# Kernel optimization log

Hardware: AMD Instinct MI355X
Metric: run time of the kernel (lower is better)

The kernel has to match this reference:

```python
import jax, jax.numpy as jnp
import numpy as np

POS = np.array([[0,3,0.5],[0,3,1.5],[0,3,2.5],[0,3,3.5],[0,3,4.5],[0,3,5.5],[1,0,0],[1,6,6],[2,0,6],[2,6,0],[3,0,0],[3,6,6],[4,0,6],[4,6,0],[5,0,0],[5,6,6],[6,0,6],[6,6,0],[7,0,0],[7,6,6],[8,0,6],[8,6,0],[9,0,0],[9,6,6],[10,0,6],[10,6,0],[11,0,0],[11,6,6],[12,0,6],[12,6,0],[13,0,0],[13,6,6],[14,0,6],[14,6,0],[15,0,0],[15,6,6],[16,0,6],[16,6,0],[17,0.5,0.5],[17,3,0.5],[17,5.5,0.5],[17,0.5,3],[17,3,3],[17,5.5,3],[17,0.5,5.5],[17,3,5.5],[17,5.5,5.5]], dtype=np.float32)  # (47,3) fixed buffer

B, S, D, H, FF, HID = 512, 47, 32, 4, 2048, 256

def _ln(x, w, b, eps=1e-5):
    mu = jnp.mean(x, -1, keepdims=True)
    var = jnp.mean((x - mu) ** 2, -1, keepdims=True)
    return (x - mu) * jax.lax.rsqrt(var + eps) * w + b

def _encoder_layer(h, wi, bi, wo, bo, l1w, l1b, f1w, f1b, f2w, f2b, l2w, l2b):
    # torch post-norm TransformerEncoderLayer; batch_first=False => attention over axis 0
    L, N, E = h.shape
    Dh = E // H
    qkv = h @ wi.T + bi                                  # (L,N,3E)
    q, k, v = jnp.split(qkv, 3, axis=-1)
    q = q.reshape(L, N, H, Dh); k = k.reshape(L, N, H, Dh); v = v.reshape(L, N, H, Dh)
    scores = jnp.einsum('lnhd,mnhd->nhlm', q, k) * (1.0 / np.sqrt(Dh))  # (N,H,L,L)
    a = jax.nn.softmax(scores, axis=-1)
    o = jnp.einsum('nhlm,mnhd->lnhd', a, v).reshape(L, N, E)
    h = _ln(h + (o @ wo.T + bo), l1w, l1b)
    ff = jax.nn.relu(h @ f1w.T + f1b) @ f2w.T + f2b
    return _ln(h + ff, l2w, l2b)

def setup_inputs():
    key = jax.random.key(0)
    ks = list(jax.random.split(key, 24))
    rn = lambda k, s, sc=0.05: jax.random.normal(k, s, jnp.float32) * sc
    return dict(
        x=jax.random.normal(ks[0], (B, S), jnp.float32),
        w_in=rn(ks[1], (D, 1)), b_in=rn(ks[2], (D,)),
        w_pos=rn(ks[3], (D, 3)), b_pos=rn(ks[4], (D,)),
        cls_token=rn(ks[5], (1, 1, D), 1.0),
        attn_in_w=rn(ks[6], (2, 3 * D, D)), attn_in_b=rn(ks[7], (2, 3 * D)),
        attn_out_w=rn(ks[8], (2, D, D)), attn_out_b=rn(ks[9], (2, D)),
        ln1_w=jnp.ones((2, D)), ln1_b=jnp.zeros((2, D)),
        ff1_w=rn(ks[10], (2, FF, D)), ff1_b=rn(ks[11], (2, FF)),
        ff2_w=rn(ks[12], (2, D, FF)), ff2_b=rn(ks[13], (2, D)),
        ln2_w=jnp.ones((2, D)), ln2_b=jnp.zeros((2, D)),
        out_w=rn(ks[14], (1, D)), out_b=rn(ks[15], (1,)),
        mlp_w0=rn(ks[16], (HID, S)), mlp_b0=rn(ks[17], (HID,)),
        mlp_w1=rn(ks[18], (HID, HID)), mlp_b1=rn(ks[19], (HID,)),
        mlp_w2=rn(ks[20], (1, HID)), mlp_b2=rn(ks[21], (1,)),
    )

def reference(x, w_in, b_in, w_pos, b_pos, cls_token, attn_in_w, attn_in_b, attn_out_w, attn_out_b, ln1_w, ln1_b, ff1_w, ff1_b, ff2_w, ff2_b, ln2_w, ln2_b, out_w, out_b, mlp_w0, mlp_b0, mlp_w1, mlp_b1, mlp_w2, mlp_b2):
    Bn = x.shape[0]
    h = x[..., None] * w_in[:, 0] + b_in                 # Linear(1,D): (B,S,D)
    h = h + (jnp.asarray(POS) @ w_pos.T + b_pos)         # pos projection (S,D)
    cls = jnp.broadcast_to(cls_token, (Bn, 1, D))
    h = jnp.concatenate([cls, h], axis=1)                # (B,S+1,D)
    for i in range(2):
        h = _encoder_layer(h, attn_in_w[i], attn_in_b[i], attn_out_w[i], attn_out_b[i], ln1_w[i], ln1_b[i], ff1_w[i], ff1_b[i], ff2_w[i], ff2_b[i], ln2_w[i], ln2_b[i])
    out = jax.nn.relu(h[:, 1:, :] @ out_w.T + out_b)[..., 0]   # (B,S); dropout = eval identity
    o = jax.nn.relu(out @ mlp_w0.T + mlp_b0)
    o = jax.nn.relu(o @ mlp_w1.T + mlp_b1)
    o = jax.nn.relu(o @ mlp_w2.T + mlp_b2)               # MLP ends with ReLU per source
    return o
```

## Files before the change

### kernel.cpp

```cpp
#include <hip/hip_runtime.h>

#define NB 512
#define NS 47
#define NP 48
#define DIM 32
#define NFF 2048
#define NHID 256
#define NROWS (NB * NP)

#define VSTR 520
#define PSTR 72
#define USTR 136

typedef _Float16 f16x8 __attribute__((ext_vector_type(8)));
typedef _Float16 f16x4 __attribute__((ext_vector_type(4)));
typedef float f32x4 __attribute__((ext_vector_type(4)));

__constant__ float POSC[NS * 3] = {
  0,3,0.5f, 0,3,1.5f, 0,3,2.5f, 0,3,3.5f, 0,3,4.5f, 0,3,5.5f,
  1,0,0, 1,6,6, 2,0,6, 2,6,0, 3,0,0, 3,6,6, 4,0,6, 4,6,0,
  5,0,0, 5,6,6, 6,0,6, 6,6,0, 7,0,0, 7,6,6, 8,0,6, 8,6,0,
  9,0,0, 9,6,6, 10,0,6, 10,6,0, 11,0,0, 11,6,6, 12,0,6, 12,6,0,
  13,0,0, 13,6,6, 14,0,6, 14,6,0, 15,0,0, 15,6,6, 16,0,6, 16,6,0,
  17,0.5f,0.5f, 17,3,0.5f, 17,5.5f,0.5f, 17,0.5f,3, 17,3,3, 17,5.5f,3,
  17,0.5f,5.5f, 17,3,5.5f, 17,5.5f,5.5f
};

__global__ __launch_bounds__(256) void prep16_kernel(const float* __restrict__ w1,
                                                     const float* __restrict__ w2,
                                                     _Float16* __restrict__ w1h,
                                                     _Float16* __restrict__ w2h) {
  int idx = blockIdx.x * 256 + threadIdx.x;
  w1h[idx] = (_Float16)w1[idx];
  w2h[idx] = (_Float16)w2[idx];
}

__global__ __launch_bounds__(256) void embed_kernel(
    const float* __restrict__ x, const float* __restrict__ w_in, const float* __restrict__ b_in,
    const float* __restrict__ w_pos, const float* __restrict__ b_pos,
    const float* __restrict__ cls, float* __restrict__ h) {
  int idx = blockIdx.x * 256 + threadIdx.x;
  int r = idx >> 5, d = idx & 31;
  int l = r / NP, n = r - l * NP;
  float v;
  if (n == 0) {
    v = cls[d];
  } else {
    int s = n - 1;
    v = x[l * NS + s] * w_in[d] + b_in[d]
      + POSC[s * 3 + 0] * w_pos[d * 3 + 0]
      + POSC[s * 3 + 1] * w_pos[d * 3 + 1]
      + POSC[s * 3 + 2] * w_pos[d * 3 + 2] + b_pos[d];
  }
  h[idx] = v;
}

__global__ __launch_bounds__(256) void kv_kernel(
    const float* __restrict__ h, const float* __restrict__ wi, const float* __restrict__ bi,
    _Float16* __restrict__ Kp, _Float16* __restrict__ Vt) {
  __shared__ float ws_[512];
  __shared__ float bs_[16];
  const int t = threadIdx.x;
  const int nh = blockIdx.x >> 1;
  const int n = nh >> 2, hh = nh & 3;
  const int l = ((blockIdx.x & 1) << 8) | t;
  for (int i = t; i < 512; i += 256) {
    int sub = i >> 8, rem = i & 255;
    int jj = rem >> 5, d = rem & 31;
    ws_[i] = wi[((sub + 1) * 32 + hh * 8 + jj) * 32 + d];
  }
  if (t < 16) bs_[t] = bi[((t >> 3) + 1) * 32 + hh * 8 + (t & 7)];
  __syncthreads();
  const float4* hrow = (const float4*)(h + (l * NP + n) * 32);
  float4 hv[8];
  #pragma unroll
  for (int i = 0; i < 8; ++i) hv[i] = hrow[i];
  f16x8 kh, kl_, vh;
  #pragma unroll
  for (int jj = 0; jj < 8; ++jj) {
    float k0 = bs_[jj], k1 = 0.f, k2 = 0.f, k3 = 0.f;
    float v0 = bs_[8 + jj], v1 = 0.f, v2 = 0.f, v3 = 0.f;
    #pragma unroll
    for (int d4 = 0; d4 < 8; ++d4) {
      float4 hvv = hv[d4];
      k0 += hvv.x * ws_[jj * 32 + 4 * d4 + 0];
      k1 += hvv.y * ws_[jj * 32 + 4 * d4 + 1];
      k2 += hvv.z * ws_[jj * 32 + 4 * d4 + 2];
      k3 += hvv.w * ws_[jj * 32 + 4 * d4 + 3];
      v0 += hvv.x * ws_[256 + jj * 32 + 4 * d4 + 0];
      v1 += hvv.y * ws_[256 + jj * 32 + 4 * d4 + 1];
      v2 += hvv.z * ws_[256 + jj * 32 + 4 * d4 + 2];
      v3 += hvv.w * ws_[256 + jj * 32 + 4 * d4 + 3];
    }
    float kv = (k0 + k1) + (k2 + k3);
    float vv = (v0 + v1) + (v2 + v3);
    kh[jj] = (_Float16)kv; kl_[jj] = (_Float16)(kv - (float)kh[jj]);
    vh[jj] = (_Float16)vv;
  }
  _Float16* kdst = Kp + ((size_t)nh * 512 + l) * 16;
  *(f16x8*)(kdst) = kh;
  *(f16x8*)(kdst + 8) = kl_;
  #pragma unroll
  for (int d = 0; d < 8; ++d) Vt[(size_t)nh * 4096 + d * 512 + l] = vh[d];
}

__global__ __launch_bounds__(256, 2) void attn_mfma_kernel(
    const float* __restrict__ h, const float* __restrict__ wi, const float* __restrict__ bi,
    const _Float16* __restrict__ Kp, const _Float16* __restrict__ Vt,
    float* __restrict__ o) {
  __shared__ alignas(16) _Float16 khi[512 * 8];
  __shared__ alignas(16) _Float16 klo[512 * 8];
  __shared__ alignas(16) _Float16 vts[8 * VSTR];
  __shared__ alignas(16) float hq_pls[2304];
  __shared__ alignas(16) _Float16 qf[64 * 16];
  __shared__ float wsq[256];
  __shared__ float bq[8];
  const int bx = blockIdx.x;
  const int nh = bx >> 3, qc = bx & 7;
  const int n = nh >> 2, hh = nh & 3;
  const int t = threadIdx.x;
  const int lane = t & 63, wv = t >> 6;
  const int c = lane & 15, g = lane >> 4;

  const _Float16* kg = Kp + (size_t)nh * 8192;
  for (int r = t; r < 512; r += 256) {
    const uint4* src = (const uint4*)(kg + r * 16);
    uint4 a = src[0], b = src[1];
    *(uint4*)(khi + r * 8) = a;
    *(uint4*)(klo + r * 8) = b;
  }
  {
    const _Float16* vg = Vt + (size_t)nh * 4096;
    for (int i = t; i < 512; i += 256) {
      int d = i >> 6, seg = i & 63;
      *(uint4*)(vts + d * VSTR + seg * 8) = *(const uint4*)(vg + d * 512 + seg * 8);
    }
  }
  wsq[t] = wi[(hh * 8 + (t & 7)) * 32 + (t >> 3)];
  if (t < 8) bq[t] = bi[hh * 8 + t];
  float* hq = hq_pls;
  {
    int row = t >> 2, quar = t & 3;
    const float4* src = (const float4*)(h + (((qc * 64 + row) * NP) + n) * 32 + quar * 8);
    *(float4*)(hq + row * 36 + quar * 8) = src[0];
    *(float4*)(hq + row * 36 + quar * 8 + 4) = src[1];
  }
  __syncthreads();

  {
    int row = t >> 2, pr = t & 3;
    #pragma unroll
    for (int u = 0; u < 2; ++u) {
      int jj = pr * 2 + u;
      float a = bq[jj];
      #pragma unroll
      for (int d = 0; d < 32; ++d) a += hq[row * 36 + d] * wsq[d * 8 + jj];
      _Float16 qh = (_Float16)a;
      _Float16 ql = (_Float16)(a - (float)qh);
      qf[row * 16 + jj] = qh;
      qf[row * 16 + 8 + jj] = ql;
    }
  }
  __syncthreads();

  const f16x8 hz = {(_Float16)0,(_Float16)0,(_Float16)0,(_Float16)0,
                    (_Float16)0,(_Float16)0,(_Float16)0,(_Float16)0};
  const f32x4 zf = {0.f, 0.f, 0.f, 0.f};
  _Float16* pls_ = (_Float16*)hq_pls;
  _Float16* myp = pls_ + wv * (16 * PSTR);
  const int q0 = qc * 64 + wv * 16;

  f16x8 aq = hz;
  if (g < 3) aq = *(const f16x8*)(qf + (wv * 16 + c) * 16 + (g & 1) * 8);

  f32x4 acc = {0.f, 0.f, 0.f, 0.f};
  float lsum[4] = {0.f, 0.f, 0.f, 0.f};

  for (int ch = 0; ch < 8; ++ch) {
    const int kb = ch * 64;
    #pragma unroll
    for (int kt = 0; kt < 4; ++kt) {
      f16x8 bk = hz;
      if (g < 2)       bk = *(const f16x8*)(khi + (kb + kt * 16 + c) * 8);
      else if (g == 2) bk = *(const f16x8*)(klo + (kb + kt * 16 + c) * 8);
      f32x4 s = __builtin_amdgcn_mfma_f32_16x16x32_f16(aq, bk, zf, 0, 0, 0);
      #pragma unroll
      for (int r = 0; r < 4; ++r) {
        float p = __expf(s[r] * 0.35355339059327373f - 2.0f);
        _Float16 ph = (_Float16)p;
        lsum[r] += (float)ph;
        myp[(g * 4 + r) * PSTR + kt * 16 + c] = ph;
      }
    }
    #pragma unroll
    for (int half = 0; half < 2; ++half) {
      f16x8 ap = *(const f16x8*)(myp + c * PSTR + half * 32 + g * 8);
      f16x8 bv = hz;
      if (c < 8) bv = *(const f16x8*)(vts + c * VSTR + kb + half * 32 + g * 8);
      acc = __builtin_amdgcn_mfma_f32_16x16x32_f16(ap, bv, acc, 0, 0, 0);
    }
  }
  #pragma unroll
  for (int m = 1; m < 16; m <<= 1) {
    #pragma unroll
    for (int r = 0; r < 4; ++r) lsum[r] += __shfl_xor(lsum[r], m, 64);
  }
  if (c < 8) {
    #pragma unroll
    for (int r = 0; r < 4; ++r) {
      float val = acc[r] / lsum[r];
      o[((q0 + g * 4 + r) * NP + n) * 32 + hh * 8 + c] = val;
    }
  }
}

__global__ __launch_bounds__(256) void proj_ln1_kernel(
    const float* __restrict__ o, const float* __restrict__ wo, const float* __restrict__ bo,
    const float* __restrict__ lw, const float* __restrict__ lb, float* __restrict__ h) {
  __shared__ float wos[32 * 33];
  __shared__ float pre[64 * 33];
  const int g = blockIdx.x, t = threadIdx.x;
  for (int i = t; i < 1024; i += 256) wos[(i >> 5) * 33 + (i & 31)] = wo[i];
  __syncthreads();
  const int subr = t >> 2, jq = t & 3;
  const int r = g * 64 + subr;
  const float4* orow = (const float4*)(o + r * 32);
  float4 ov[8];
  #pragma unroll
  for (int i = 0; i < 8; ++i) ov[i] = orow[i];
  const float* hres = h + r * 32 + jq * 8;
  #pragma unroll
  for (int jj = 0; jj < 8; ++jj) {
    int j = jq * 8 + jj;
    float a0 = bo[j], a1 = 0.f, a2 = 0.f, a3 = 0.f;
    #pragma unroll
    for (int d4 = 0; d4 < 8; ++d4) {
      float4 vv = ov[d4];
      a0 += vv.x * wos[j * 33 + 4 * d4 + 0];
      a1 += vv.y * wos[j * 33 + 4 * d4 + 1];
      a2 += vv.z * wos[j * 33 + 4 * d4 + 2];
      a3 += vv.w * wos[j * 33 + 4 * d4 + 3];
    }
    pre[subr * 33 + j] = (a0 + a1) + (a2 + a3) + hres[jj];
  }
  __syncthreads();
  if (t < 64) {
    float mu = 0.f;
    #pragma unroll
    for (int d = 0; d < 32; ++d) mu += pre[t * 33 + d];
    mu *= (1.f / 32.f);
    float var = 0.f;
    #pragma unroll
    for (int d = 0; d < 32; ++d) { float dv = pre[t * 33 + d] - mu; var += dv * dv; }
    float rs = rsqrtf(var * (1.f / 32.f) + 1e-5f);
    float* hrow = h + (g * 64 + t) * 32;
    #pragma unroll
    for (int d = 0; d < 32; ++d)
      hrow[d] = (pre[t * 33 + d] - mu) * rs * lw[d] + lb[d];
  }
}

__global__ __launch_bounds__(256) void ff_fused_kernel(
    const float* __restrict__ h, const _Float16* __restrict__ w1h,
    const float* __restrict__ b1, const _Float16* __restrict__ w2h,
    const float* __restrict__ b2, const float* __restrict__ lw,
    const float* __restrict__ lb, const float* __restrict__ ow,
    const float* __restrict__ ob, float* __restrict__ svec, int do_svec) {
  __shared__ alignas(16) _Float16 ubuf[4][2][16 * USTR];
  __shared__ alignas(16) float yw[4][32 * 33];
  const int t = threadIdx.x;
  const int lane = t & 63;
  const int wv = t >> 6;
  const int nl = lane & 15;
  const int g = lane >> 4;
  const int g4 = g * 4;
  const int r0 = blockIdx.x * 32;

  f16x8 hfrag[2];
  #pragma unroll
  for (int tt = 0; tt < 2; ++tt) {
    const float4 h0 = *(const float4*)(h + (r0 + tt * 16 + nl) * 32 + g * 8);
    const float4 h1 = *(const float4*)(h + (r0 + tt * 16 + nl) * 32 + g * 8 + 4);
    hfrag[tt][0] = (_Float16)h0.x; hfrag[tt][1] = (_Float16)h0.y;
    hfrag[tt][2] = (_Float16)h0.z; hfrag[tt][3] = (_Float16)h0.w;
    hfrag[tt][4] = (_Float16)h1.x; hfrag[tt][5] = (_Float16)h1.y;
    hfrag[tt][6] = (_Float16)h1.z; hfrag[tt][7] = (_Float16)h1.w;
  }

  f32x4 acc00 = {0.f,0.f,0.f,0.f}, acc01 = {0.f,0.f,0.f,0.f};
  f32x4 acc10 = {0.f,0.f,0.f,0.f}, acc11 = {0.f,0.f,0.f,0.f};
  const f32x4 zero = {0.f, 0.f, 0.f, 0.f};
  const int ffbase = wv * 512;

  #pragma unroll
  for (int sc = 0; sc < 4; ++sc) {
    const int ffb = ffbase + sc * 128;
    f16x8 wf[8];
    #pragma unroll
    for (int ft = 0; ft < 8; ++ft)
      wf[ft] = *(const f16x8*)(w1h + (ffb + ft * 16 + nl) * 32 + g * 8);
    f32x4 cc0[8], cc1[8];
    #pragma unroll
    for (int ft = 0; ft < 8; ++ft) {
      cc0[ft] = __builtin_amdgcn_mfma_f32_16x16x32_f16(wf[ft], hfrag[0], zero, 0, 0, 0);
      cc1[ft] = __builtin_amdgcn_mfma_f32_16x16x32_f16(wf[ft], hfrag[1], zero, 0, 0, 0);
    }
    #pragma unroll
    for (int ft = 0; ft < 8; ++ft) {
      float4 bv = *(const float4*)(b1 + ffb + ft * 16 + g4);
      f16x4 u0, u1;
      u0[0] = (_Float16)fmaxf(cc0[ft][0] + bv.x, 0.f);
      u0[1] = (_Float16)fmaxf(cc0[ft][1] + bv.y, 0.f);
      u0[2] = (_Float16)fmaxf(cc0[ft][2] + bv.z, 0.f);
      u0[3] = (_Float16)fmaxf(cc0[ft][3] + bv.w, 0.f);
      u1[0] = (_Float16)fmaxf(cc1[ft][0] + bv.x, 0.f);
      u1[1] = (_Float16)fmaxf(cc1[ft][1] + bv.y, 0.f);
      u1[2] = (_Float16)fmaxf(cc1[ft][2] + bv.z, 0.f);
      u1[3] = (_Float16)fmaxf(cc1[ft][3] + bv.w, 0.f);
      *(f16x4*)(ubuf[wv][0] + nl * USTR + ft * 16 + g4) = u0;
      *(f16x4*)(ubuf[wv][1] + nl * USTR + ft * 16 + g4) = u1;
    }
    f16x8 w2f0[4], w2f1[4];
    #pragma unroll
    for (int kk = 0; kk < 4; ++kk) {
      w2f0[kk] = *(const f16x8*)(w2h + nl * NFF + ffb + kk * 32 + g * 8);
      w2f1[kk] = *(const f16x8*)(w2h + (16 + nl) * NFF + ffb + kk * 32 + g * 8);
    }
    #pragma unroll
    for (int kk = 0; kk < 4; ++kk) {
      f16x8 uf0 = *(const f16x8*)(ubuf[wv][0] + nl * USTR + kk * 32 + g * 8);
      f16x8 uf1 = *(const f16x8*)(ubuf[wv][1] + nl * USTR + kk * 32 + g * 8);
      acc00 = __builtin_amdgcn_mfma_f32_16x16x32_f16(uf0, w2f0[kk], acc00, 0, 0, 0);
      acc01 = __builtin_amdgcn_mfma_f32_16x16x32_f16(uf0, w2f1[kk], acc01, 0, 0, 0);
      acc10 = __builtin_amdgcn_mfma_f32_16x16x32_f16(uf1, w2f0[kk], acc10, 0, 0, 0);
      acc11 = __builtin_amdgcn_mfma_f32_16x16x32_f16(uf1, w2f1[kk], acc11, 0, 0, 0);
    }
  }
  #pragma unroll
  for (int r = 0; r < 4; ++r) {
    yw[wv][(g4 + r) * 33 + nl]      = acc00[r];
    yw[wv][(g4 + r) * 33 + 16 + nl] = acc01[r];
    yw[wv][(16 + g4 + r) * 33 + nl]      = acc10[r];
    yw[wv][(16 + g4 + r) * 33 + 16 + nl] = acc11[r];
  }
  __syncthreads();

  float* pre = (float*)ubuf;
  {
    int idx = t;
    #pragma unroll
    for (int u = 0; u < 4; ++u, idx += 256) {
      int tok = idx >> 5, d = idx & 31;
      int off = tok * 33 + d;
      float v = yw[0][off] + yw[1][off] + yw[2][off] + yw[3][off]
              + b2[d] + h[(r0 + tok) * 32 + d];
      pre[off] = v;
    }
  }
  __syncthreads();

  if (t < 32) {
    float mu = 0.f;
    #pragma unroll
    for (int d = 0; d < 32; ++d) mu += pre[t * 33 + d];
    mu *= (1.f / 32.f);
    float var = 0.f;
    #pragma unroll
    for (int d = 0; d < 32; ++d) { float dv = pre[t * 33 + d] - mu; var += dv * dv; }
    float rs = rsqrtf(var * (1.f / 32.f) + 1e-5f);
    const int rr = r0 + t;
    float* hrow = (float*)h + (size_t)rr * 32;
    float hn[32];
    #pragma unroll
    for (int d = 0; d < 32; ++d) {
      hn[d] = (pre[t * 33 + d] - mu) * rs * lw[d] + lb[d];
      hrow[d] = hn[d];
    }
    if (do_svec) {
      int l = rr / NP, n = rr - l * NP;
      if (n > 0) {
        float a = ob[0];
        #pragma unroll
        for (int d = 0; d < 32; ++d) a += hn[d] * ow[d];
        svec[l * NS + (n - 1)] = fmaxf(a, 0.f);
      }
    }
  }
}

__global__ __launch_bounds__(256) void head_kernel(
    const float* __restrict__ svec,
    const float* __restrict__ m0w, const float* __restrict__ m0b,
    const float* __restrict__ m1w, const float* __restrict__ m1b,
    const float* __restrict__ m2w, const float* __restrict__ m2b,
    float* __restrict__ out) {
  __shared__ float sv[NS];
  __shared__ float hid[NHID];
  __shared__ float red[4];
  const int l = blockIdx.x, t = threadIdx.x;
  if (t < NS) sv[t] = svec[l * NS + t];
  __syncthreads();
  {
    float a = m0b[t];
    const float* wr = m0w + t * NS;
    #pragma unroll
    for (int s = 0; s < NS; ++s) a += sv[s] * wr[s];
    hid[t] = fmaxf(a, 0.f);
  }
  __syncthreads();
  {
    float a = m1b[t];
    const float4* wr = (const float4*)(m1w + t * NHID);
    #pragma unroll 8
    for (int j4 = 0; j4 < 64; ++j4) {
      float4 w = wr[j4];
      a += hid[4 * j4 + 0] * w.x + hid[4 * j4 + 1] * w.y
         + hid[4 * j4 + 2] * w.z + hid[4 * j4 + 3] * w.w;
    }
    float h2 = fmaxf(a, 0.f);
    float part = h2 * m2w[t];
    #pragma unroll
    for (int off = 32; off > 0; off >>= 1) part += __shfl_down(part, off, 64);
    if ((t & 63) == 0) red[t >> 6] = part;
  }
  __syncthreads();
  if (t == 0) out[l] = fmaxf(red[0] + red[1] + red[2] + red[3] + m2b[0], 0.f);
}

extern "C" void kernel_launch(void* const* d_in, const int* in_sizes, int n_in,
                              void* d_out, int out_size, void* d_ws, size_t ws_size,
                              hipStream_t stream) {
  (void)in_sizes; (void)n_in; (void)out_size; (void)ws_size;
  const float* x     = (const float*)d_in[0];
  const float* w_in  = (const float*)d_in[1];
  const float* b_in  = (const float*)d_in[2];
  const float* w_pos = (const float*)d_in[3];
  const float* b_pos = (const float*)d_in[4];
  const float* cls   = (const float*)d_in[5];
  const float* wi    = (const float*)d_in[6];
  const float* bi    = (const float*)d_in[7];
  const float* wo    = (const float*)d_in[8];
  const float* bo    = (const float*)d_in[9];
  const float* l1w   = (const float*)d_in[10];
  const float* l1b   = (const float*)d_in[11];
  const float* f1w   = (const float*)d_in[12];
  const float* f1b   = (const float*)d_in[13];
  const float* f2w   = (const float*)d_in[14];
  const float* f2b   = (const float*)d_in[15];
  const float* l2w   = (const float*)d_in[16];
  const float* l2b   = (const float*)d_in[17];
  const float* ow    = (const float*)d_in[18];
  const float* ob    = (const float*)d_in[19];
  const float* m0w   = (const float*)d_in[20];
  const float* m0b   = (const float*)d_in[21];
  const float* m1w   = (const float*)d_in[22];
  const float* m1b   = (const float*)d_in[23];
  const float* m2w   = (const float*)d_in[24];
  const float* m2b   = (const float*)d_in[25];
  float* out = (float*)d_out;

  float* ws   = (float*)d_ws;
  float* h    = ws;
  float* o    = ws + 786432;
  float* R2   = ws + 1572864;
  _Float16* Kp = (_Float16*)R2;
  _Float16* Vt = (_Float16*)(R2 + 786432);
  float* svec = ws + 2752512;
  _Float16* w1h = (_Float16*)(ws + 2776576);
  _Float16* w2h = (_Float16*)(ws + 2842112);

  prep16_kernel<<<512, 256, 0, stream>>>(f1w, f2w, w1h, w2h);
  embed_kernel<<<3072, 256, 0, stream>>>(x, w_in, b_in, w_pos, b_pos, cls, h);
  for (int L = 0; L < 2; ++L) {
    kv_kernel<<<384, 256, 0, stream>>>(h, wi + L * 3072, bi + L * 96, Kp, Vt);
    attn_mfma_kernel<<<1536, 256, 0, stream>>>(h, wi + L * 3072, bi + L * 96, Kp, Vt, o);
    proj_ln1_kernel<<<384, 256, 0, stream>>>(o, wo + L * 1024, bo + L * 32,
                                             l1w + L * 32, l1b + L * 32, h);
    ff_fused_kernel<<<768, 256, 0, stream>>>(h, w1h + L * 65536, f1b + L * NFF,
                                             w2h + L * 65536, f2b + L * 32,
                                             l2w + L * 32, l2b + L * 32,
                                             ow, ob, svec, L);
  }
  head_kernel<<<512, 256, 0, stream>>>(svec, m0w, m0b, m1w, m1b, m2w, m2b, out);
}
```

Measured before the change: 171.8 us.

## Process more queries per attention block and more tokens per FF block

The attention kernel now handles 128 query rows per block in two passes, so each staged K/V tile in shared memory is reused twice and the grid is halved. The feed-forward kernel processes 48 tokens per block instead of 32, so each loaded W1/W2 fragment and bias feeds three token tiles, and it reuses double-buffered ubuf slots in an interleaved per-tile loop. This cuts the weight and K/V loads per unit of work, at the cost of fewer blocks (768 and 512), more shared memory for yw, and higher register pressure, which may reduce occupancy.

```diff
diff --git a/kernel.cpp b/kernel.cpp
--- a/kernel.cpp
+++ b/kernel.cpp
@@ -7,6 +7,7 @@
 #define NFF 2048
 #define NHID 256
 #define NROWS (NB * NP)
+#define FTOK 48
 
 #define VSTR 520
 #define PSTR 72
@@ -112,11 +113,11 @@
   __shared__ alignas(16) _Float16 klo[512 * 8];
   __shared__ alignas(16) _Float16 vts[8 * VSTR];
   __shared__ alignas(16) float hq_pls[2304];
-  __shared__ alignas(16) _Float16 qf[64 * 16];
+  __shared__ alignas(16) _Float16 qf[128 * 16];
   __shared__ float wsq[256];
   __shared__ float bq[8];
   const int bx = blockIdx.x;
-  const int nh = bx >> 3, qc = bx & 7;
+  const int nh = bx >> 2, qc = bx & 3;
   const int n = nh >> 2, hh = nh & 3;
   const int t = threadIdx.x;
   const int lane = t & 63, wv = t >> 6;
@@ -139,77 +140,85 @@
   wsq[t] = wi[(hh * 8 + (t & 7)) * 32 + (t >> 3)];
   if (t < 8) bq[t] = bi[hh * 8 + t];
   float* hq = hq_pls;
-  {
-    int row = t >> 2, quar = t & 3;
-    const float4* src = (const float4*)(h + (((qc * 64 + row) * NP) + n) * 32 + quar * 8);
-    *(float4*)(hq + row * 36 + quar * 8) = src[0];
-    *(float4*)(hq + row * 36 + quar * 8 + 4) = src[1];
-  }
-  __syncthreads();
-
-  {
-    int row = t >> 2, pr = t & 3;
-    #pragma unroll
-    for (int u = 0; u < 2; ++u) {
-      int jj = pr * 2 + u;
-      float a = bq[jj];
-      #pragma unroll
-      for (int d = 0; d < 32; ++d) a += hq[row * 36 + d] * wsq[d * 8 + jj];
-      _Float16 qh = (_Float16)a;
-      _Float16 ql = (_Float16)(a - (float)qh);
-      qf[row * 16 + jj] = qh;
-      qf[row * 16 + 8 + jj] = ql;
-    }
-  }
-  __syncthreads();
+
+  #pragma unroll
+  for (int rp = 0; rp < 2; ++rp) {
+    {
+      int row = t >> 2, quar = t & 3;
+      const float4* src =
+          (const float4*)(h + (((qc * 128 + rp * 64 + row) * NP) + n) * 32 + quar * 8);
+      float4 a = src[0], b = src[1];
+      __syncthreads();
+      *(float4*)(hq + row * 36 + quar * 8) = a;
+      *(float4*)(hq + row * 36 + quar * 8 + 4) = b;
+    }
+    __syncthreads();
+    {
+      int row = t >> 2, pr = t & 3;
+      #pragma unroll
+      for (int u = 0; u < 2; ++u) {
+        int jj = pr * 2 + u;
+        float a = bq[jj];
+        #pragma unroll
+        for (int d = 0; d < 32; ++d) a += hq[row * 36 + d] * wsq[d * 8 + jj];
+        _Float16 qh = (_Float16)a;
+        _Float16 ql = (_Float16)(a - (float)qh);
+        qf[(rp * 64 + row) * 16 + jj] = qh;
+        qf[(rp * 64 + row) * 16 + 8 + jj] = ql;
+      }
+    }
+    __syncthreads();
+  }
 
   const f16x8 hz = {(_Float16)0,(_Float16)0,(_Float16)0,(_Float16)0,
                     (_Float16)0,(_Float16)0,(_Float16)0,(_Float16)0};
   const f32x4 zf = {0.f, 0.f, 0.f, 0.f};
   _Float16* pls_ = (_Float16*)hq_pls;
   _Float16* myp = pls_ + wv * (16 * PSTR);
-  const int q0 = qc * 64 + wv * 16;
-
-  f16x8 aq = hz;
-  if (g < 3) aq = *(const f16x8*)(qf + (wv * 16 + c) * 16 + (g & 1) * 8);
-
-  f32x4 acc = {0.f, 0.f, 0.f, 0.f};
-  float lsum[4] = {0.f, 0.f, 0.f, 0.f};
-
-  for (int ch = 0; ch < 8; ++ch) {
-    const int kb = ch * 64;
-    #pragma unroll
-    for (int kt = 0; kt < 4; ++kt) {
-      f16x8 bk = hz;
-      if (g < 2)       bk = *(const f16x8*)(khi + (kb + kt * 16 + c) * 8);
-      else if (g == 2) bk = *(const f16x8*)(klo + (kb + kt * 16 + c) * 8);
-      f32x4 s = __builtin_amdgcn_mfma_f32_16x16x32_f16(aq, bk, zf, 0, 0, 0);
+
+  #pragma unroll
+  for (int pass = 0; pass < 2; ++pass) {
+    const int q0 = qc * 128 + pass * 64 + wv * 16;
+    f16x8 aq = hz;
+    if (g < 3) aq = *(const f16x8*)(qf + (pass * 64 + wv * 16 + c) * 16 + (g & 1) * 8);
+    f32x4 acc = {0.f, 0.f, 0.f, 0.f};
+    float lsum[4] = {0.f, 0.f, 0.f, 0.f};
+
+    for (int ch = 0; ch < 8; ++ch) {
+      const int kb = ch * 64;
+      #pragma unroll
+      for (int kt = 0; kt < 4; ++kt) {
+        f16x8 bk = hz;
+        if (g < 2)       bk = *(const f16x8*)(khi + (kb + kt * 16 + c) * 8);
+        else if (g == 2) bk = *(const f16x8*)(klo + (kb + kt * 16 + c) * 8);
+        f32x4 s = __builtin_amdgcn_mfma_f32_16x16x32_f16(aq, bk, zf, 0, 0, 0);
+        #pragma unroll
+        for (int r = 0; r < 4; ++r) {
+          float p = __expf(s[r] * 0.35355339059327373f - 2.0f);
+          _Float16 ph = (_Float16)p;
+          lsum[r] += (float)ph;
+          myp[(g * 4 + r) * PSTR + kt * 16 + c] = ph;
+        }
+      }
+      #pragma unroll
+      for (int half = 0; half < 2; ++half) {
+        f16x8 ap = *(const f16x8*)(myp + c * PSTR + half * 32 + g * 8);
+        f16x8 bv = hz;
+        if (c < 8) bv = *(const f16x8*)(vts + c * VSTR + kb + half * 32 + g * 8);
+        acc = __builtin_amdgcn_mfma_f32_16x16x32_f16(ap, bv, acc, 0, 0, 0);
+      }
+    }
+    #pragma unroll
+    for (int m = 1; m < 16; m <<= 1) {
+      #pragma unroll
+      for (int r = 0; r < 4; ++r) lsum[r] += __shfl_xor(lsum[r], m, 64);
+    }
+    if (c < 8) {
       #pragma unroll
       for (int r = 0; r < 4; ++r) {
-        float p = __expf(s[r] * 0.35355339059327373f - 2.0f);
-        _Float16 ph = (_Float16)p;
-        lsum[r] += (float)ph;
-        myp[(g * 4 + r) * PSTR + kt * 16 + c] = ph;
-      }
-    }
-    #pragma unroll
-    for (int half = 0; half < 2; ++half) {
-      f16x8 ap = *(const f16x8*)(myp + c * PSTR + half * 32 + g * 8);
-      f16x8 bv = hz;
-      if (c < 8) bv = *(const f16x8*)(vts + c * VSTR + kb + half * 32 + g * 8);
-      acc = __builtin_amdgcn_mfma_f32_16x16x32_f16(ap, bv, acc, 0, 0, 0);
-    }
-  }
-  #pragma unroll
-  for (int m = 1; m < 16; m <<= 1) {
-    #pragma unroll
-    for (int r = 0; r < 4; ++r) lsum[r] += __shfl_xor(lsum[r], m, 64);
-  }
-  if (c < 8) {
-    #pragma unroll
-    for (int r = 0; r < 4; ++r) {
-      float val = acc[r] / lsum[r];
-      o[((q0 + g * 4 + r) * NP + n) * 32 + hh * 8 + c] = val;
+        float val = acc[r] / lsum[r];
+        o[((q0 + g * 4 + r) * NP + n) * 32 + hh * 8 + c] = val;
+      }
     }
   }
 }
@@ -267,18 +276,18 @@
     const float* __restrict__ lb, const float* __restrict__ ow,
     const float* __restrict__ ob, float* __restrict__ svec, int do_svec) {
   __shared__ alignas(16) _Float16 ubuf[4][2][16 * USTR];
-  __shared__ alignas(16) float yw[4][32 * 33];
+  __shared__ alignas(16) float yw[4][FTOK * 33];
   const int t = threadIdx.x;
   const int lane = t & 63;
   const int wv = t >> 6;
   const int nl = lane & 15;
   const int g = lane >> 4;
   const int g4 = g * 4;
-  const int r0 = blockIdx.x * 32;
-
-  f16x8 hfrag[2];
-  #pragma unroll
-  for (int tt = 0; tt < 2; ++tt) {
+  const int r0 = blockIdx.x * FTOK;
+
+  f16x8 hfrag[3];
+  #pragma unroll
+  for (int tt = 0; tt < 3; ++tt) {
     const float4 h0 = *(const float4*)(h + (r0 + tt * 16 + nl) * 32 + g * 8);
     const float4 h1 = *(const float4*)(h + (r0 + tt * 16 + nl) * 32 + g * 8 + 4);
     hfrag[tt][0] = (_Float16)h0.x; hfrag[tt][1] = (_Float16)h0.y;
@@ -287,8 +296,8 @@
     hfrag[tt][6] = (_Float16)h1.z; hfrag[tt][7] = (_Float16)h1.w;
   }
 
-  f32x4 acc00 = {0.f,0.f,0.f,0.f}, acc01 = {0.f,0.f,0.f,0.f};
-  f32x4 acc10 = {0.f,0.f,0.f,0.f}, acc11 = {0.f,0.f,0.f,0.f};
+  f32x4 acc0[3] = {{0.f,0.f,0.f,0.f},{0.f,0.f,0.f,0.f},{0.f,0.f,0.f,0.f}};
+  f32x4 acc1[3] = {{0.f,0.f,0.f,0.f},{0.f,0.f,0.f,0.f},{0.f,0.f,0.f,0.f}};
   const f32x4 zero = {0.f, 0.f, 0.f, 0.f};
   const int ffbase = wv * 512;
 
@@ -296,29 +305,11 @@
   for (int sc = 0; sc < 4; ++sc) {
     const int ffb = ffbase + sc * 128;
     f16x8 wf[8];
-    #pragma unroll
-    for (int ft = 0; ft < 8; ++ft)
+    float4 bv[8];
+    #pragma unroll
+    for (int ft = 0; ft < 8; ++ft) {
       wf[ft] = *(const f16x8*)(w1h + (ffb + ft * 16 + nl) * 32 + g * 8);
-    f32x4 cc0[8], cc1[8];
-    #pragma unroll
-    for (int ft = 0; ft < 8; ++ft) {
-      cc0[ft] = __builtin_amdgcn_mfma_f32_16x16x32_f16(wf[ft], hfrag[0], zero, 0, 0, 0);
-      cc1[ft] = __builtin_amdgcn_mfma_f32_16x16x32_f16(wf[ft], hfrag[1], zero, 0, 0, 0);
-    }
-    #pragma unroll
-    for (int ft = 0; ft < 8; ++ft) {
-      float4 bv = *(const float4*)(b1 + ffb + ft * 16 + g4);
-      f16x4 u0, u1;
-      u0[0] = (_Float16)fmaxf(cc0[ft][0] + bv.x, 0.f);
-      u0[1] = (_Float16)fmaxf(cc0[ft][1] + bv.y, 0.f);
-      u0[2] = (_Float16)fmaxf(cc0[ft][2] + bv.z, 0.f);
-      u0[3] = (_Float16)fmaxf(cc0[ft][3] + bv.w, 0.f);
-      u1[0] = (_Float16)fmaxf(cc1[ft][0] + bv.x, 0.f);
-      u1[1] = (_Float16)fmaxf(cc1[ft][1] + bv.y, 0.f);
-      u1[2] = (_Float16)fmaxf(cc1[ft][2] + bv.z, 0.f);
-      u1[3] = (_Float16)fmaxf(cc1[ft][3] + bv.w, 0.f);
-      *(f16x4*)(ubuf[wv][0] + nl * USTR + ft * 16 + g4) = u0;
-      *(f16x4*)(ubuf[wv][1] + nl * USTR + ft * 16 + g4) = u1;
+      bv[ft] = *(const float4*)(b1 + ffb + ft * 16 + g4);
     }
     f16x8 w2f0[4], w2f1[4];
     #pragma unroll
@@ -327,21 +318,36 @@
       w2f1[kk] = *(const f16x8*)(w2h + (16 + nl) * NFF + ffb + kk * 32 + g * 8);
     }
     #pragma unroll
-    for (int kk = 0; kk < 4; ++kk) {
-      f16x8 uf0 = *(const f16x8*)(ubuf[wv][0] + nl * USTR + kk * 32 + g * 8);
-      f16x8 uf1 = *(const f16x8*)(ubuf[wv][1] + nl * USTR + kk * 32 + g * 8);
-      acc00 = __builtin_amdgcn_mfma_f32_16x16x32_f16(uf0, w2f0[kk], acc00, 0, 0, 0);
-      acc01 = __builtin_amdgcn_mfma_f32_16x16x32_f16(uf0, w2f1[kk], acc01, 0, 0, 0);
-      acc10 = __builtin_amdgcn_mfma_f32_16x16x32_f16(uf1, w2f0[kk], acc10, 0, 0, 0);
-      acc11 = __builtin_amdgcn_mfma_f32_16x16x32_f16(uf1, w2f1[kk], acc11, 0, 0, 0);
-    }
-  }
-  #pragma unroll
-  for (int r = 0; r < 4; ++r) {
-    yw[wv][(g4 + r) * 33 + nl]      = acc00[r];
-    yw[wv][(g4 + r) * 33 + 16 + nl] = acc01[r];
-    yw[wv][(16 + g4 + r) * 33 + nl]      = acc10[r];
-    yw[wv][(16 + g4 + r) * 33 + 16 + nl] = acc11[r];
+    for (int tt = 0; tt < 3; ++tt) {
+      _Float16* ub = ubuf[wv][tt & 1];
+      f32x4 cc[8];
+      #pragma unroll
+      for (int ft = 0; ft < 8; ++ft)
+        cc[ft] = __builtin_amdgcn_mfma_f32_16x16x32_f16(wf[ft], hfrag[tt], zero, 0, 0, 0);
+      #pragma unroll
+      for (int ft = 0; ft < 8; ++ft) {
+        f16x4 uv;
+        uv[0] = (_Float16)fmaxf(cc[ft][0] + bv[ft].x, 0.f);
+        uv[1] = (_Float16)fmaxf(cc[ft][1] + bv[ft].y, 0.f);
+        uv[2] = (_Float16)fmaxf(cc[ft][2] + bv[ft].z, 0.f);
+        uv[3] = (_Float16)fmaxf(cc[ft][3] + bv[ft].w, 0.f);
+        *(f16x4*)(ub + nl * USTR + ft * 16 + g4) = uv;
+      }
+      #pragma unroll
+      for (int kk = 0; kk < 4; ++kk) {
+        f16x8 uf = *(const f16x8*)(ub + nl * USTR + kk * 32 + g * 8);
+        acc0[tt] = __builtin_amdgcn_mfma_f32_16x16x32_f16(uf, w2f0[kk], acc0[tt], 0, 0, 0);
+        acc1[tt] = __builtin_amdgcn_mfma_f32_16x16x32_f16(uf, w2f1[kk], acc1[tt], 0, 0, 0);
+      }
+    }
+  }
+  #pragma unroll
+  for (int tt = 0; tt < 3; ++tt) {
+    #pragma unroll
+    for (int r = 0; r < 4; ++r) {
+      yw[wv][(tt * 16 + g4 + r) * 33 + nl]      = acc0[tt][r];
+      yw[wv][(tt * 16 + g4 + r) * 33 + 16 + nl] = acc1[tt][r];
+    }
   }
   __syncthreads();
 
@@ -349,7 +355,7 @@
   {
     int idx = t;
     #pragma unroll
-    for (int u = 0; u < 4; ++u, idx += 256) {
+    for (int u = 0; u < 6; ++u, idx += 256) {
       int tok = idx >> 5, d = idx & 31;
       int off = tok * 33 + d;
       float v = yw[0][off] + yw[1][off] + yw[2][off] + yw[3][off]
@@ -359,7 +365,7 @@
   }
   __syncthreads();
 
-  if (t < 32) {
+  if (t < FTOK) {
     float mu = 0.f;
     #pragma unroll
     for (int d = 0; d < 32; ++d) mu += pre[t * 33 + d];
@@ -473,10 +479,10 @@
   embed_kernel<<<3072, 256, 0, stream>>>(x, w_in, b_in, w_pos, b_pos, cls, h);
   for (int L = 0; L < 2; ++L) {
     kv_kernel<<<384, 256, 0, stream>>>(h, wi + L * 3072, bi + L * 96, Kp, Vt);
-    attn_mfma_kernel<<<1536, 256, 0, stream>>>(h, wi + L * 3072, bi + L * 96, Kp, Vt, o);
+    attn_mfma_kernel<<<768, 256, 0, stream>>>(h, wi + L * 3072, bi + L * 96, Kp, Vt, o);
     proj_ln1_kernel<<<384, 256, 0, stream>>>(o, wo + L * 1024, bo + L * 32,
                                              l1w + L * 32, l1b + L * 32, h);
-    ff_fused_kernel<<<768, 256, 0, stream>>>(h, w1h + L * 65536, f1b + L * NFF,
+    ff_fused_kernel<<<512, 256, 0, stream>>>(h, w1h + L * 65536, f1b + L * NFF,
                                              w2h + L * 65536, f2b + L * 32,
                                              l2w + L * 32, l2b + L * 32,
                                              ow, ob, svec, L);
```

After: 163.9 us. -4.6%, faster.
